# Kernel optimization log

Measured on AMD Instinct MI355X. Metric: run time of the kernel, lower is better.

Reference implementation:

```python
import jax, jax.numpy as jnp
import numpy as np

EMBED_DIM = 1024
NUM_HEADS = 16
HEAD_DIM = EMBED_DIM // NUM_HEADS
SCALING = HEAD_DIM ** -0.5
W_SCALE = 0.02  # small init so exp(scores) in focused path stays finite


def setup_inputs() -> dict:
    key = jax.random.key(0)
    ks = jax.random.split(key, 12)
    B, T = 2, 2048
    hidden_states = jax.random.normal(ks[0], (B, T, EMBED_DIM), dtype=jnp.float32)
    focused_attention = jax.random.uniform(ks[1], (B, T, T), dtype=jnp.float32)
    def lin(kw, kb):
        W = jax.random.normal(kw, (EMBED_DIM, EMBED_DIM), dtype=jnp.float32) * W_SCALE
        b = jax.random.normal(kb, (EMBED_DIM,), dtype=jnp.float32) * W_SCALE
        return W, b
    Wq, bq = lin(ks[2], ks[3])
    Wk, bk = lin(ks[4], ks[5])
    Wv, bv = lin(ks[6], ks[7])
    Wo, bo = lin(ks[8], ks[9])
    return {"hidden_states": hidden_states, "focused_attention": focused_attention,
            "Wq": Wq, "bq": bq, "Wk": Wk, "bk": bk, "Wv": Wv, "bv": bv, "Wo": Wo, "bo": bo}


def reference(hidden_states, focused_attention, Wq, bq, Wk, bk, Wv, bv, Wo, bo):
    B, T, D = hidden_states.shape
    H, hd = NUM_HEADS, HEAD_DIM

    def shape_heads(x):  # [B,T,D] -> [B,H,T,hd]
        return x.reshape(B, T, H, hd).transpose(0, 2, 1, 3)

    q = shape_heads((hidden_states @ Wq.T + bq) * SCALING)
    k = shape_heads(hidden_states @ Wk.T + bk)
    v = shape_heads(hidden_states @ Wv.T + bv)

    # [B,H,T,S] raw attention logits
    scores = jnp.einsum('bhtd,bhsd->bhts', q, k)

    # focused_attention path: exp-weighted normalization (not a plain softmax)
    f = focused_attention[:, None, :, :]  # broadcast over heads
    e = f * jnp.exp(scores)
    attn = e / jnp.sum(e, axis=-1, keepdims=True)

    out = jnp.einsum('bhts,bhsd->bhtd', attn, v)  # [B,H,T,hd]
    out = out.transpose(0, 2, 1, 3).reshape(B, T, D)
    return out @ Wo.T + bo
```

## Files before the change

kernel.cpp:

```cpp
#include <hip/hip_runtime.h>
#include <stdint.h>


typedef __attribute__((ext_vector_type(8))) short short8;
typedef __attribute__((ext_vector_type(4))) short short4v;
typedef __attribute__((ext_vector_type(4))) float f32x4;
typedef unsigned short u16;

#define T_SEQ 2048
#define NH    16
#define HD    64
#define DM    1024

__device__ __forceinline__ float b2f(u16 h) {
  union { unsigned u; float f; } v; v.u = ((unsigned)h) << 16; return v.f;
}
__device__ __forceinline__ u16 f2bf(float x) {
  union { float f; unsigned u; } v; v.f = x;
  unsigned r = v.u + 0x7fffu + ((v.u >> 16) & 1u);
  return (u16)(r >> 16);
}
__device__ __forceinline__ short8 cvt8(const float* p) {
  const f32x4 a = *(const f32x4*)p;
  const f32x4 b = *(const f32x4*)(p + 4);
  short8 o;
  o[0] = (short)f2bf(a[0]); o[1] = (short)f2bf(a[1]);
  o[2] = (short)f2bf(a[2]); o[3] = (short)f2bf(a[3]);
  o[4] = (short)f2bf(b[0]); o[5] = (short)f2bf(b[1]);
  o[6] = (short)f2bf(b[2]); o[7] = (short)f2bf(b[3]);
  return o;
}
__device__ __forceinline__ void gl_lds16(const void* g, void* l) {
  __builtin_amdgcn_global_load_lds(
      (const __attribute__((address_space(1))) void*)g,
      (__attribute__((address_space(3))) void*)l, 16, 0, 0);
}

#define HS_CH 524288u
#define F_CH  1048576u
#define W_CH  131072u
__global__ void cvt_kernel(const float* __restrict__ hs, const float* __restrict__ f,
                           const float* __restrict__ Wq, const float* __restrict__ Wk,
                           const float* __restrict__ Wv, const float* __restrict__ Wo,
                           u16* __restrict__ hsb, u16* __restrict__ fb,
                           u16* __restrict__ Wqb, u16* __restrict__ Wkb,
                           u16* __restrict__ Wvb, u16* __restrict__ Wob) {
  unsigned c = blockIdx.x * 256 + threadIdx.x;
  const float* s; u16* d; unsigned off;
  if (c < HS_CH)                       { s = hs; d = hsb; off = c; }
  else if ((c -= HS_CH) < F_CH)        { s = f;  d = fb;  off = c; }
  else if ((c -= F_CH) < W_CH)         { s = Wq; d = Wqb; off = c; }
  else if ((c -= W_CH) < W_CH)         { s = Wk; d = Wkb; off = c; }
  else if ((c -= W_CH) < W_CH)         { s = Wv; d = Wvb; off = c; }
  else                                 { s = Wo; d = Wob; off = c - W_CH; }
  *(short8*)&d[(size_t)off * 8] = cvt8(&s[(size_t)off * 8]);
}

__global__ __launch_bounds__(256, 4) void qkv_kernel(
    const void* __restrict__ Xv,
    const void* __restrict__ Wqv, const float* __restrict__ bq,
    const void* __restrict__ Wkv, const float* __restrict__ bk,
    const void* __restrict__ Wvv, const float* __restrict__ bv,
    int isf32,
    u16* __restrict__ q, u16* __restrict__ k, u16* __restrict__ v)
{
  const int z = blockIdx.z;
  const void* Wp = (z == 0) ? Wqv : (z == 1) ? Wkv : Wvv;
  const float* bias = (z == 0) ? bq : (z == 1) ? bk : bv;

  __shared__ alignas(16) short lsA[4][128][8];
  __shared__ alignas(16) short lsB[4][128][8];

  const int tid = threadIdx.x;
  const int lane = tid & 63;
  const int wv = tid >> 6;
  const int lq = lane >> 4, li = lane & 15;
  const int wm = wv >> 1, wn = wv & 1;

  const int m0 = blockIdx.y * 128;
  const int n0 = blockIdx.x * 128;

  f32x4 acc[4][4];
#pragma unroll
  for (int i = 0; i < 4; i++)
#pragma unroll
    for (int j = 0; j < 4; j++) acc[i][j] = (f32x4){0.f, 0.f, 0.f, 0.f};

  for (int k0 = 0; k0 < DM; k0 += 32) {
    if (isf32) {
      const float* X32 = (const float*)Xv;
      const float* W32 = (const float*)Wp;
#pragma unroll
      for (int r = 0; r < 2; ++r) {
        const int idx = tid + 256 * r;
        const int row = idx >> 2, slab = idx & 3;
        *(short8*)&lsA[slab][row][0] = cvt8(&X32[(size_t)(m0 + row) * DM + k0 + slab * 8]);
        *(short8*)&lsB[slab][row][0] = cvt8(&W32[(size_t)(n0 + row) * DM + k0 + slab * 8]);
      }
    } else {
      const u16* X16 = (const u16*)Xv;
      const u16* W16 = (const u16*)Wp;
#pragma unroll
      for (int r = 0; r < 2; ++r) {
        const int row = r * 64 + lane;
        gl_lds16(&X16[(size_t)(m0 + row) * DM + k0 + wv * 8], &lsA[wv][row][0]);
        gl_lds16(&W16[(size_t)(n0 + row) * DM + k0 + wv * 8], &lsB[wv][row][0]);
      }
    }
    __syncthreads();
    short8 af[4], bf[4];
#pragma unroll
    for (int mt = 0; mt < 4; ++mt)
      af[mt] = *(const short8*)&lsA[lq][wm * 64 + mt * 16 + li][0];
#pragma unroll
    for (int nt = 0; nt < 4; ++nt)
      bf[nt] = *(const short8*)&lsB[lq][wn * 64 + nt * 16 + li][0];
#pragma unroll
    for (int mt = 0; mt < 4; ++mt)
#pragma unroll
      for (int nt = 0; nt < 4; ++nt)
        acc[mt][nt] = __builtin_amdgcn_mfma_f32_16x16x32_bf16(af[mt], bf[nt], acc[mt][nt], 0, 0, 0);
    __syncthreads();
  }

  float bs[4];
#pragma unroll
  for (int nt = 0; nt < 4; ++nt) bs[nt] = bias[n0 + wn * 64 + nt * 16 + li];
  const float scale = (z == 0) ? 0.125f : 1.0f;

  if (z != 2) {
    u16* dst = (z == 0) ? q : k;
#pragma unroll
    for (int mt = 0; mt < 4; ++mt) {
      const int mbase = m0 + wm * 64 + mt * 16 + lq * 4;
#pragma unroll
      for (int nt = 0; nt < 4; ++nt) {
        const int n = n0 + wn * 64 + nt * 16 + li;
        const int h = n >> 6, d = n & 63;
#pragma unroll
        for (int r = 0; r < 4; ++r) {
          const int m = mbase + r;
          const int b = m >> 11, t = m & (T_SEQ - 1);
          dst[((size_t)(b * NH + h) * T_SEQ + t) * HD + d] = f2bf((acc[mt][nt][r] + bs[nt]) * scale);
        }
      }
    }
  } else {
#pragma unroll
    for (int mt = 0; mt < 4; ++mt) {
      const int mbase = m0 + wm * 64 + mt * 16 + lq * 4;
      const int b = mbase >> 11, t = mbase & (T_SEQ - 1);
#pragma unroll
      for (int nt = 0; nt < 4; ++nt) {
        const int n = n0 + wn * 64 + nt * 16 + li;
        const int h = n >> 6, d = n & 63;
        u16 pk[4];
#pragma unroll
        for (int r = 0; r < 4; ++r) pk[r] = f2bf(acc[mt][nt][r] + bs[nt]);
        *(short4v*)&v[((size_t)(b * NH + h) * HD + d) * T_SEQ + t] = *(const short4v*)pk;
      }
    }
  }
}

__global__ __launch_bounds__(256, 2) void attn_kernel(
    const u16* __restrict__ q, const u16* __restrict__ k,
    const u16* __restrict__ v, const void* __restrict__ fv,
    int isf32, u16* __restrict__ ao)
{
  __shared__ alignas(16) u16 Kl[2][8192];
  __shared__ alignas(16) u16 Vl[2][8192];
  __shared__ alignas(16) u16 pPf[4][2048];

  const int tid = threadIdx.x;
  const int w = tid >> 6;
  const int lane = tid & 63;
  const int lq = lane >> 4, li = lane & 15;

  const int t0 = blockIdx.x * 128;
  const int h = blockIdx.y;
  const int b = blockIdx.z;

  const u16* qh = q + (size_t)(b * NH + h) * T_SEQ * HD;
  const u16* kh = k + (size_t)(b * NH + h) * T_SEQ * HD;
  const u16* vh = v + (size_t)(b * NH + h) * HD * T_SEQ;

  short8 qf[2][2];
#pragma unroll
  for (int g = 0; g < 2; ++g)
#pragma unroll
    for (int kk = 0; kk < 2; ++kk)
      qf[g][kk] = *(const short8*)&qh[(size_t)(t0 + w * 32 + g * 16 + li) * HD + kk * 32 + lq * 8];

  f32x4 oacc[2][4];
#pragma unroll
  for (int g = 0; g < 2; ++g)
#pragma unroll
    for (int j = 0; j < 4; j++) oacc[g][j] = (f32x4){0.f, 0.f, 0.f, 0.f};
  float den[2] = {0.f, 0.f};

#define STAGE_TILE(S0, BUF)                                                      \
  {                                                                              \
    const u16* gK = kh + (size_t)(S0) * HD;                                      \
    const u16* gV = vh + (S0);                                                   \
    u16* Kb = &Kl[BUF][0];                                                       \
    u16* Vb = &Vl[BUF][0];                                                       \
    _Pragma("unroll")                                                            \
    for (int r = 0; r < 4; ++r) {                                                \
      const int L = (w * 4 + r) * 64 + lane;                                     \
      const int sl = L >> 3, jx = L & 7, j = jx ^ (sl & 7);                      \
      gl_lds16(gK + (size_t)sl * HD + j * 8, Kb + (size_t)L * 8);                \
      const int d = L >> 4, scx = L & 15, sc = scx ^ (d & 15);                   \
      gl_lds16(gV + (size_t)d * T_SEQ + sc * 8, Vb + (size_t)L * 8);             \
    }                                                                            \
  }

  STAGE_TILE(0, 0)
  __syncthreads();

  for (int it = 0; it < 16; ++it) {
    const int cur = it & 1;
    const int s0 = it * 128;
    if (it < 15) STAGE_TILE(s0 + 128, cur ^ 1)

    const u16* Kb = &Kl[cur][0];
    const u16* Vb = &Vl[cur][0];

    short8 kf[2][8];
#pragma unroll
    for (int kk = 0; kk < 2; ++kk)
#pragma unroll
      for (int mt = 0; mt < 8; ++mt) {
        const int sl = mt * 16 + li;
        const int c = sl * 8 + ((kk * 4 + lq) ^ (sl & 7));
        kf[kk][mt] = *(const short8*)&Kb[(size_t)c * 8];
      }
    short8 vf[4][4];
#pragma unroll
    for (int kk = 0; kk < 4; ++kk)
#pragma unroll
      for (int dn = 0; dn < 4; ++dn) {
        const int d = dn * 16 + li;
        const int c = d * 16 + ((kk * 4 + lq) ^ (d & 15));
        vf[kk][dn] = *(const short8*)&Vb[(size_t)c * 8];
      }

    u16* pw = &pPf[w][0];
#pragma unroll
    for (int g = 0; g < 2; ++g) {
      f32x4 sacc[8];
#pragma unroll
      for (int mt = 0; mt < 8; ++mt) sacc[mt] = (f32x4){0.f, 0.f, 0.f, 0.f};
#pragma unroll
      for (int kk = 0; kk < 2; ++kk)
#pragma unroll
        for (int mt = 0; mt < 8; ++mt)
          sacc[mt] = __builtin_amdgcn_mfma_f32_16x16x32_bf16(kf[kk][mt], qf[g][kk], sacc[mt], 0, 0, 0);

      const int tg = t0 + w * 32 + g * 16 + li;
#pragma unroll
      for (int mt = 0; mt < 8; ++mt) {
        u16 pk[4];
        if (isf32) {
          const float* fb = (const float*)fv + (size_t)b * T_SEQ * T_SEQ;
          const f32x4 fr = *(const f32x4*)&fb[(size_t)tg * T_SEQ + s0 + mt * 16 + lq * 4];
#pragma unroll
          for (int r = 0; r < 4; ++r) {
            const float e = __expf(fminf(sacc[mt][r], 60.0f));
            const float p = fr[r] * e;
            den[g] += p;
            pk[r] = f2bf(p);
          }
        } else {
          const u16* fb = (const u16*)fv + (size_t)b * T_SEQ * T_SEQ;
          const short4v fr = *(const short4v*)&fb[(size_t)tg * T_SEQ + s0 + mt * 16 + lq * 4];
#pragma unroll
          for (int r = 0; r < 4; ++r) {
            const float e = __expf(fminf(sacc[mt][r], 60.0f));
            const float p = b2f((u16)fr[r]) * e;
            den[g] += p;
            pk[r] = f2bf(p);
          }
        }
        const int c8 = (mt * 4 + lq) ^ ((li & 7) << 1);
        *(short4v*)&pw[li * 128 + c8 * 4] = *(const short4v*)pk;
      }

#pragma unroll
      for (int kk = 0; kk < 4; ++kk) {
        const int c8 = ((kk << 3) + (lq << 1)) ^ ((li & 7) << 1);
        const short8 pf = *(const short8*)&pw[li * 128 + c8 * 4];
#pragma unroll
        for (int dn = 0; dn < 4; ++dn)
          oacc[g][dn] = __builtin_amdgcn_mfma_f32_16x16x32_bf16(pf, vf[kk][dn], oacc[g][dn], 0, 0, 0);
      }
    }
    __syncthreads();
  }

#pragma unroll
  for (int g = 0; g < 2; ++g) {
    den[g] += __shfl_xor(den[g], 16, 64);
    den[g] += __shfl_xor(den[g], 32, 64);
  }

#pragma unroll
  for (int g = 0; g < 2; ++g) {
#pragma unroll
    for (int r = 0; r < 4; ++r) {
      const float rd = 1.0f / __shfl(den[g], lq * 4 + r, 64);
      const int t = t0 + w * 32 + g * 16 + lq * 4 + r;
#pragma unroll
      for (int dn = 0; dn < 4; ++dn)
        ao[(size_t)(b * T_SEQ + t) * DM + h * HD + dn * 16 + li] = f2bf(oacc[g][dn][r] * rd);
    }
  }
#undef STAGE_TILE
}

__global__ __launch_bounds__(256, 4) void oproj_kernel(
    const u16* __restrict__ A, const void* __restrict__ Wov,
    const float* __restrict__ bo, int isf32, float* __restrict__ out)
{
  __shared__ alignas(16) short lsA[4][128][8];
  __shared__ alignas(16) short lsB[4][128][8];

  const int tid = threadIdx.x;
  const int lane = tid & 63;
  const int wv = tid >> 6;
  const int lq = lane >> 4, li = lane & 15;
  const int wm = wv >> 1, wn = wv & 1;

  const int m0 = blockIdx.y * 128;
  const int n0 = blockIdx.x * 128;

  f32x4 acc[4][4];
#pragma unroll
  for (int i = 0; i < 4; i++)
#pragma unroll
    for (int j = 0; j < 4; j++) acc[i][j] = (f32x4){0.f, 0.f, 0.f, 0.f};

  for (int k0 = 0; k0 < DM; k0 += 32) {
#pragma unroll
    for (int r = 0; r < 2; ++r) {
      const int row = r * 64 + lane;
      gl_lds16(&A[(size_t)(m0 + row) * DM + k0 + wv * 8], &lsA[wv][row][0]);
    }
    if (isf32) {
      const float* W32 = (const float*)Wov;
#pragma unroll
      for (int r = 0; r < 2; ++r) {
        const int idx = tid + 256 * r;
        const int row = idx >> 2, slab = idx & 3;
        *(short8*)&lsB[slab][row][0] = cvt8(&W32[(size_t)(n0 + row) * DM + k0 + slab * 8]);
      }
    } else {
      const u16* W16 = (const u16*)Wov;
#pragma unroll
      for (int r = 0; r < 2; ++r) {
        const int row = r * 64 + lane;
        gl_lds16(&W16[(size_t)(n0 + row) * DM + k0 + wv * 8], &lsB[wv][row][0]);
      }
    }
    __syncthreads();
    short8 af[4], bf[4];
#pragma unroll
    for (int mt = 0; mt < 4; ++mt)
      af[mt] = *(const short8*)&lsA[lq][wm * 64 + mt * 16 + li][0];
#pragma unroll
    for (int nt = 0; nt < 4; ++nt)
      bf[nt] = *(const short8*)&lsB[lq][wn * 64 + nt * 16 + li][0];
#pragma unroll
    for (int mt = 0; mt < 4; ++mt)
#pragma unroll
      for (int nt = 0; nt < 4; ++nt)
        acc[mt][nt] = __builtin_amdgcn_mfma_f32_16x16x32_bf16(af[mt], bf[nt], acc[mt][nt], 0, 0, 0);
    __syncthreads();
  }

  float bs[4];
#pragma unroll
  for (int nt = 0; nt < 4; ++nt) bs[nt] = bo[n0 + wn * 64 + nt * 16 + li];

#pragma unroll
  for (int mt = 0; mt < 4; ++mt) {
    const int mbase = m0 + wm * 64 + mt * 16 + lq * 4;
#pragma unroll
    for (int nt = 0; nt < 4; ++nt) {
      const int n = n0 + wn * 64 + nt * 16 + li;
#pragma unroll
      for (int r = 0; r < 4; ++r)
        out[(size_t)(mbase + r) * DM + n] = acc[mt][nt][r] + bs[nt];
    }
  }
}

extern "C" void kernel_launch(void* const* d_in, const int* in_sizes, int n_in,
                              void* d_out, int out_size, void* d_ws, size_t ws_size,
                              hipStream_t stream) {
  (void)in_sizes; (void)n_in; (void)out_size;
  const float* hs = (const float*)d_in[0];
  const float* fa = (const float*)d_in[1];
  const float* Wq = (const float*)d_in[2];
  const float* bq = (const float*)d_in[3];
  const float* Wk = (const float*)d_in[4];
  const float* bk = (const float*)d_in[5];
  const float* Wv = (const float*)d_in[6];
  const float* bv = (const float*)d_in[7];
  const float* Wo = (const float*)d_in[8];
  const float* bo = (const float*)d_in[9];
  float* out = (float*)d_out;

  const size_t NEED = 256 + 2u * (8388608u + 4194304u + 4u * 1048576u + 4u * 4194304u);
  char* base = (char*)d_ws + 256;
  if (ws_size >= NEED) {
    u16* fb  = (u16*)base;
    u16* hsb = fb + 8388608u;
    u16* Wqb = hsb + 4194304u;
    u16* Wkb = Wqb + 1048576u;
    u16* Wvb = Wkb + 1048576u;
    u16* Wob = Wvb + 1048576u;
    u16* qw  = Wob + 1048576u;
    u16* kw  = qw + 4194304u;
    u16* vw  = kw + 4194304u;
    u16* aw  = vw + 4194304u;
    cvt_kernel<<<8192, 256, 0, stream>>>(hs, fa, Wq, Wk, Wv, Wo, hsb, fb, Wqb, Wkb, Wvb, Wob);
    qkv_kernel<<<dim3(8, 32, 3), 256, 0, stream>>>(hsb, Wqb, bq, Wkb, bk, Wvb, bv, 0, qw, kw, vw);
    attn_kernel<<<dim3(16, 16, 2), 256, 0, stream>>>(qw, kw, vw, fb, 0, aw);
    oproj_kernel<<<dim3(8, 32, 1), 256, 0, stream>>>(aw, Wob, bo, 0, out);
  } else {
    u16* qw = (u16*)base;
    u16* kw = qw + 4194304u;
    u16* vw = kw + 4194304u;
    u16* aw = vw + 4194304u;
    qkv_kernel<<<dim3(8, 32, 3), 256, 0, stream>>>(hs, Wq, bq, Wk, bk, Wv, bv, 1, qw, kw, vw);
    attn_kernel<<<dim3(16, 16, 2), 256, 0, stream>>>(qw, kw, vw, fa, 1, aw);
    oproj_kernel<<<dim3(8, 32, 1), 256, 0, stream>>>(aw, Wo, bo, 1, out);
  }
}
```

Before: 341.8 us.

## Restructure QKV/attention layouts, stage V and output writes through LDS, prefetch focus

```diff
diff --git a/kernel.cpp b/kernel.cpp
--- a/kernel.cpp
+++ b/kernel.cpp
@@ -68,8 +68,9 @@
   const void* Wp = (z == 0) ? Wqv : (z == 1) ? Wkv : Wvv;
   const float* bias = (z == 0) ? bq : (z == 1) ? bk : bv;
 
-  __shared__ alignas(16) short lsA[4][128][8];
-  __shared__ alignas(16) short lsB[4][128][8];
+  __shared__ alignas(16) u16 smem[17408];
+  u16* lsA = smem;
+  u16* lsB = smem + 4096;
 
   const int tid = threadIdx.x;
   const int lane = tid & 63;
@@ -94,8 +95,8 @@
       for (int r = 0; r < 2; ++r) {
         const int idx = tid + 256 * r;
         const int row = idx >> 2, slab = idx & 3;
-        *(short8*)&lsA[slab][row][0] = cvt8(&X32[(size_t)(m0 + row) * DM + k0 + slab * 8]);
-        *(short8*)&lsB[slab][row][0] = cvt8(&W32[(size_t)(n0 + row) * DM + k0 + slab * 8]);
+        *(short8*)&lsA[(slab * 128 + row) * 8] = cvt8(&X32[(size_t)(m0 + row) * DM + k0 + slab * 8]);
+        *(short8*)&lsB[(slab * 128 + row) * 8] = cvt8(&W32[(size_t)(n0 + row) * DM + k0 + slab * 8]);
       }
     } else {
       const u16* X16 = (const u16*)Xv;
@@ -103,18 +104,18 @@
 #pragma unroll
       for (int r = 0; r < 2; ++r) {
         const int row = r * 64 + lane;
-        gl_lds16(&X16[(size_t)(m0 + row) * DM + k0 + wv * 8], &lsA[wv][row][0]);
-        gl_lds16(&W16[(size_t)(n0 + row) * DM + k0 + wv * 8], &lsB[wv][row][0]);
+        gl_lds16(&X16[(size_t)(m0 + row) * DM + k0 + wv * 8], &lsA[(wv * 128 + row) * 8]);
+        gl_lds16(&W16[(size_t)(n0 + row) * DM + k0 + wv * 8], &lsB[(wv * 128 + row) * 8]);
       }
     }
     __syncthreads();
     short8 af[4], bf[4];
 #pragma unroll
     for (int mt = 0; mt < 4; ++mt)
-      af[mt] = *(const short8*)&lsA[lq][wm * 64 + mt * 16 + li][0];
+      af[mt] = *(const short8*)&lsA[(lq * 128 + wm * 64 + mt * 16 + li) * 8];
 #pragma unroll
     for (int nt = 0; nt < 4; ++nt)
-      bf[nt] = *(const short8*)&lsB[lq][wn * 64 + nt * 16 + li][0];
+      bf[nt] = *(const short8*)&lsB[(lq * 128 + wn * 64 + nt * 16 + li) * 8];
 #pragma unroll
     for (int mt = 0; mt < 4; ++mt)
 #pragma unroll
@@ -126,9 +127,9 @@
   float bs[4];
 #pragma unroll
   for (int nt = 0; nt < 4; ++nt) bs[nt] = bias[n0 + wn * 64 + nt * 16 + li];
-  const float scale = (z == 0) ? 0.125f : 1.0f;
 
   if (z != 2) {
+    const float scale = (z == 0) ? 0.125f : 1.0f;
     u16* dst = (z == 0) ? q : k;
 #pragma unroll
     for (int mt = 0; mt < 4; ++mt) {
@@ -136,29 +137,35 @@
 #pragma unroll
       for (int nt = 0; nt < 4; ++nt) {
         const int n = n0 + wn * 64 + nt * 16 + li;
-        const int h = n >> 6, d = n & 63;
-#pragma unroll
-        for (int r = 0; r < 4; ++r) {
-          const int m = mbase + r;
-          const int b = m >> 11, t = m & (T_SEQ - 1);
-          dst[((size_t)(b * NH + h) * T_SEQ + t) * HD + d] = f2bf((acc[mt][nt][r] + bs[nt]) * scale);
-        }
+#pragma unroll
+        for (int r = 0; r < 4; ++r)
+          dst[(size_t)(mbase + r) * DM + n] = f2bf((acc[mt][nt][r] + bs[nt]) * scale);
       }
     }
   } else {
 #pragma unroll
     for (int mt = 0; mt < 4; ++mt) {
-      const int mbase = m0 + wm * 64 + mt * 16 + lq * 4;
-      const int b = mbase >> 11, t = mbase & (T_SEQ - 1);
+      const int mcol = wm * 64 + mt * 16 + lq * 4;
 #pragma unroll
       for (int nt = 0; nt < 4; ++nt) {
-        const int n = n0 + wn * 64 + nt * 16 + li;
-        const int h = n >> 6, d = n & 63;
+        const int nrow = wn * 64 + nt * 16 + li;
         u16 pk[4];
 #pragma unroll
         for (int r = 0; r < 4; ++r) pk[r] = f2bf(acc[mt][nt][r] + bs[nt]);
-        *(short4v*)&v[((size_t)(b * NH + h) * HD + d) * T_SEQ + t] = *(const short4v*)pk;
-      }
+        *(short4v*)&smem[nrow * 136 + mcol] = *(const short4v*)pk;
+      }
+    }
+    __syncthreads();
+    const int b = m0 >> 11;
+    const int t0 = m0 & (T_SEQ - 1);
+#pragma unroll
+    for (int p = 0; p < 8; ++p) {
+      const int n = p * 16 + (tid >> 4);
+      const int c = tid & 15;
+      const short8 val = *(const short8*)&smem[n * 136 + c * 8];
+      const int ng = n0 + n;
+      const int h = ng >> 6, d = ng & 63;
+      *(short8*)&v[((size_t)(b * NH + h) * HD + d) * T_SEQ + t0 + c * 8] = val;
     }
   }
 }
@@ -181,8 +188,8 @@
   const int h = blockIdx.y;
   const int b = blockIdx.z;
 
-  const u16* qh = q + (size_t)(b * NH + h) * T_SEQ * HD;
-  const u16* kh = k + (size_t)(b * NH + h) * T_SEQ * HD;
+  const u16* qh = q + (size_t)b * T_SEQ * DM + h * HD;
+  const u16* kh = k + (size_t)b * T_SEQ * DM + h * HD;
   const u16* vh = v + (size_t)(b * NH + h) * HD * T_SEQ;
 
   short8 qf[2][2];
@@ -190,7 +197,7 @@
   for (int g = 0; g < 2; ++g)
 #pragma unroll
     for (int kk = 0; kk < 2; ++kk)
-      qf[g][kk] = *(const short8*)&qh[(size_t)(t0 + w * 32 + g * 16 + li) * HD + kk * 32 + lq * 8];
+      qf[g][kk] = *(const short8*)&qh[(size_t)(t0 + w * 32 + g * 16 + li) * DM + kk * 32 + lq * 8];
 
   f32x4 oacc[2][4];
 #pragma unroll
@@ -199,9 +206,11 @@
     for (int j = 0; j < 4; j++) oacc[g][j] = (f32x4){0.f, 0.f, 0.f, 0.f};
   float den[2] = {0.f, 0.f};
 
+  const int tg0 = t0 + w * 32 + li;
+
 #define STAGE_TILE(S0, BUF)                                                      \
   {                                                                              \
-    const u16* gK = kh + (size_t)(S0) * HD;                                      \
+    const u16* gK = kh + (size_t)(S0) * DM;                                      \
     const u16* gV = vh + (S0);                                                   \
     u16* Kb = &Kl[BUF][0];                                                       \
     u16* Vb = &Vl[BUF][0];                                                       \
@@ -209,7 +218,7 @@
     for (int r = 0; r < 4; ++r) {                                                \
       const int L = (w * 4 + r) * 64 + lane;                                     \
       const int sl = L >> 3, jx = L & 7, j = jx ^ (sl & 7);                      \
-      gl_lds16(gK + (size_t)sl * HD + j * 8, Kb + (size_t)L * 8);                \
+      gl_lds16(gK + (size_t)sl * DM + j * 8, Kb + (size_t)L * 8);                \
       const int d = L >> 4, scx = L & 15, sc = scx ^ (d & 15);                   \
       gl_lds16(gV + (size_t)d * T_SEQ + sc * 8, Vb + (size_t)L * 8);             \
     }                                                                            \
@@ -223,6 +232,28 @@
     const int s0 = it * 128;
     if (it < 15) STAGE_TILE(s0 + 128, cur ^ 1)
 
+    short4v fr[2][8];
+    if (isf32) {
+      const float* f32p = (const float*)fv + (size_t)b * T_SEQ * T_SEQ;
+#pragma unroll
+      for (int g = 0; g < 2; ++g)
+#pragma unroll
+        for (int mt = 0; mt < 8; ++mt) {
+          const f32x4 fx = *(const f32x4*)&f32p[(size_t)(tg0 + g * 16) * T_SEQ + s0 + mt * 16 + lq * 4];
+          short4v pk;
+          pk[0] = (short)f2bf(fx[0]); pk[1] = (short)f2bf(fx[1]);
+          pk[2] = (short)f2bf(fx[2]); pk[3] = (short)f2bf(fx[3]);
+          fr[g][mt] = pk;
+        }
+    } else {
+      const u16* f16p = (const u16*)fv + (size_t)b * T_SEQ * T_SEQ;
+#pragma unroll
+      for (int g = 0; g < 2; ++g)
+#pragma unroll
+        for (int mt = 0; mt < 8; ++mt)
+          fr[g][mt] = *(const short4v*)&f16p[(size_t)(tg0 + g * 16) * T_SEQ + s0 + mt * 16 + lq * 4];
+    }
+
     const u16* Kb = &Kl[cur][0];
     const u16* Vb = &Vl[cur][0];
 
@@ -235,64 +266,48 @@
         const int c = sl * 8 + ((kk * 4 + lq) ^ (sl & 7));
         kf[kk][mt] = *(const short8*)&Kb[(size_t)c * 8];
       }
-    short8 vf[4][4];
-#pragma unroll
-    for (int kk = 0; kk < 4; ++kk)
-#pragma unroll
-      for (int dn = 0; dn < 4; ++dn) {
-        const int d = dn * 16 + li;
-        const int c = d * 16 + ((kk * 4 + lq) ^ (d & 15));
-        vf[kk][dn] = *(const short8*)&Vb[(size_t)c * 8];
+
+    f32x4 sacc[2][8];
+#pragma unroll
+    for (int g = 0; g < 2; ++g)
+#pragma unroll
+      for (int mt = 0; mt < 8; ++mt) sacc[g][mt] = (f32x4){0.f, 0.f, 0.f, 0.f};
+#pragma unroll
+    for (int kk = 0; kk < 2; ++kk)
+#pragma unroll
+      for (int mt = 0; mt < 8; ++mt) {
+        sacc[0][mt] = __builtin_amdgcn_mfma_f32_16x16x32_bf16(kf[kk][mt], qf[0][kk], sacc[0][mt], 0, 0, 0);
+        sacc[1][mt] = __builtin_amdgcn_mfma_f32_16x16x32_bf16(kf[kk][mt], qf[1][kk], sacc[1][mt], 0, 0, 0);
       }
 
     u16* pw = &pPf[w][0];
 #pragma unroll
     for (int g = 0; g < 2; ++g) {
-      f32x4 sacc[8];
-#pragma unroll
-      for (int mt = 0; mt < 8; ++mt) sacc[mt] = (f32x4){0.f, 0.f, 0.f, 0.f};
-#pragma unroll
-      for (int kk = 0; kk < 2; ++kk)
-#pragma unroll
-        for (int mt = 0; mt < 8; ++mt)
-          sacc[mt] = __builtin_amdgcn_mfma_f32_16x16x32_bf16(kf[kk][mt], qf[g][kk], sacc[mt], 0, 0, 0);
-
-      const int tg = t0 + w * 32 + g * 16 + li;
 #pragma unroll
       for (int mt = 0; mt < 8; ++mt) {
+        const short4v fx = fr[g][mt];
         u16 pk[4];
-        if (isf32) {
-          const float* fb = (const float*)fv + (size_t)b * T_SEQ * T_SEQ;
-          const f32x4 fr = *(const f32x4*)&fb[(size_t)tg * T_SEQ + s0 + mt * 16 + lq * 4];
-#pragma unroll
-          for (int r = 0; r < 4; ++r) {
-            const float e = __expf(fminf(sacc[mt][r], 60.0f));
-            const float p = fr[r] * e;
-            den[g] += p;
-            pk[r] = f2bf(p);
-          }
-        } else {
-          const u16* fb = (const u16*)fv + (size_t)b * T_SEQ * T_SEQ;
-          const short4v fr = *(const short4v*)&fb[(size_t)tg * T_SEQ + s0 + mt * 16 + lq * 4];
-#pragma unroll
-          for (int r = 0; r < 4; ++r) {
-            const float e = __expf(fminf(sacc[mt][r], 60.0f));
-            const float p = b2f((u16)fr[r]) * e;
-            den[g] += p;
-            pk[r] = f2bf(p);
-          }
+#pragma unroll
+        for (int r = 0; r < 4; ++r) {
+          const float e = __expf(sacc[g][mt][r]);
+          const float p = b2f((u16)fx[r]) * e;
+          den[g] += p;
+          pk[r] = f2bf(p);
         }
         const int c8 = (mt * 4 + lq) ^ ((li & 7) << 1);
         *(short4v*)&pw[li * 128 + c8 * 4] = *(const short4v*)pk;
       }
-
 #pragma unroll
       for (int kk = 0; kk < 4; ++kk) {
         const int c8 = ((kk << 3) + (lq << 1)) ^ ((li & 7) << 1);
         const short8 pf = *(const short8*)&pw[li * 128 + c8 * 4];
 #pragma unroll
-        for (int dn = 0; dn < 4; ++dn)
-          oacc[g][dn] = __builtin_amdgcn_mfma_f32_16x16x32_bf16(pf, vf[kk][dn], oacc[g][dn], 0, 0, 0);
+        for (int dn = 0; dn < 4; ++dn) {
+          const int d = dn * 16 + li;
+          const int c = d * 16 + ((kk * 4 + lq) ^ (d & 15));
+          const short8 vf = *(const short8*)&Vb[(size_t)c * 8];
+          oacc[g][dn] = __builtin_amdgcn_mfma_f32_16x16x32_bf16(pf, vf, oacc[g][dn], 0, 0, 0);
+        }
       }
     }
     __syncthreads();
@@ -304,16 +319,26 @@
     den[g] += __shfl_xor(den[g], 32, 64);
   }
 
-#pragma unroll
-  for (int g = 0; g < 2; ++g) {
+  u16* pw = &pPf[w][0];
+#pragma unroll
+  for (int g = 0; g < 2; ++g)
 #pragma unroll
     for (int r = 0; r < 4; ++r) {
       const float rd = 1.0f / __shfl(den[g], lq * 4 + r, 64);
-      const int t = t0 + w * 32 + g * 16 + lq * 4 + r;
-#pragma unroll
-      for (int dn = 0; dn < 4; ++dn)
-        ao[(size_t)(b * T_SEQ + t) * DM + h * HD + dn * 16 + li] = f2bf(oacc[g][dn][r] * rd);
-    }
+      const int trow = g * 16 + lq * 4 + r;
+#pragma unroll
+      for (int dn = 0; dn < 4; ++dn) {
+        const int d = dn * 16 + li;
+        const int ch = ((d >> 3) ^ (trow & 7));
+        pw[trow * 64 + ch * 8 + (d & 7)] = f2bf(oacc[g][dn][r] * rd);
+      }
+    }
+  const int rloc = lane >> 1, half = lane & 1;
+#pragma unroll
+  for (int c = 0; c < 4; ++c) {
+    const int ch = ((half * 4 + c) ^ (rloc & 7));
+    const short8 vv = *(const short8*)&pw[rloc * 64 + ch * 8];
+    *(short8*)&ao[(size_t)(b * T_SEQ + t0 + w * 32 + rloc) * DM + h * HD + half * 32 + c * 8] = vv;
   }
 #undef STAGE_TILE
 }
```

Result: faster. 292.9 us (-14.3%).
